# Kernel tuning notes

Hardware: AMD Instinct MI355X
Metric: run time of the kernel (lower is better)

Reference implementation:

```python
import jax, jax.numpy as jnp
import numpy as np
from jax import lax

H = 128  # rec1_size = input_size = hidden_size


def setup_inputs() -> dict:
    key = jax.random.key(0)
    ks = jax.random.split(key, 7)
    B, T = 64, 2048
    x = jax.random.normal(ks[0], (B, T, H), dtype=jnp.float32)
    h0 = jax.random.normal(ks[1], (1, B, H), dtype=jnp.float32)
    c0 = jax.random.normal(ks[2], (1, B, H), dtype=jnp.float32)
    s = 1.0 / np.sqrt(H)  # PyTorch LSTM init: U(-1/sqrt(H), 1/sqrt(H))
    W_ih = jax.random.uniform(ks[3], (4 * H, H), jnp.float32, -s, s)
    W_hh = jax.random.uniform(ks[4], (4 * H, H), jnp.float32, -s, s)
    b_ih = jax.random.uniform(ks[5], (4 * H,), jnp.float32, -s, s)
    b_hh = jax.random.uniform(ks[6], (4 * H,), jnp.float32, -s, s)
    return {"x": x, "h0": h0, "c0": c0, "W_ih": W_ih, "W_hh": W_hh,
            "b_ih": b_ih, "b_hh": b_hh}


def _lstm(x, h0, c0, W_ih, W_hh, b_ih, b_hh):
    # Precompute the input projection for all timesteps in one big GEMM.
    # Gate order in PyTorch: i, f, g, o.
    xg = jnp.einsum('bti,gi->btg', x, W_ih) + b_ih + b_hh  # [B, T, 4H]

    def step(carry, xg_t):
        h, c = carry                       # [B, H], [B, H]
        g = xg_t + h @ W_hh.T              # [B, 4H]
        i = jax.nn.sigmoid(g[:, 0 * H:1 * H])
        f = jax.nn.sigmoid(g[:, 1 * H:2 * H])
        gg = jnp.tanh(g[:, 2 * H:3 * H])
        o = jax.nn.sigmoid(g[:, 3 * H:4 * H])
        c_new = f * c + i * gg
        h_new = o * jnp.tanh(c_new)
        return (h_new, c_new), h_new

    (_, _), hs = lax.scan(step, (h0[0], c0[0]), jnp.swapaxes(xg, 0, 1))
    return jnp.swapaxes(hs, 0, 1)          # [B, T, H]


def reference(x, h0, c0, W_ih, W_hh, b_ih, b_hh):
    # The module's `activation` attribute is never applied in forward();
    # output is the raw LSTM sequence of hidden states.
    return _lstm(x, h0, c0, W_ih, W_hh, b_ih, b_hh)
```

## Files before the change

kernel.cpp:

```cpp
#include <hip/hip_runtime.h>
#include <cstdint>
#include <cmath>


#define HID 128
#define G4  512
#define BB  64
#define TT  2048

typedef float v2f __attribute__((ext_vector_type(2)));
typedef float v4f __attribute__((ext_vector_type(4)));

#define PIN2(v) asm volatile("" : "+v"(v))
#define FMA2(A, B, C) __builtin_elementwise_fma((A), (B), (C))

#define LOG2E  1.442695041f

template<int CTRL>
__device__ __forceinline__ float dpp_mov(float v) {
    return __int_as_float(__builtin_amdgcn_update_dpp(
        0, __float_as_int(v), CTRL, 0xF, 0xF, true));
}
#define BF8(p) { p += dpp_mov<0xB1>(p); p += dpp_mov<0x4E>(p); p += dpp_mov<0x141>(p); }

__global__ __launch_bounds__(512)
__attribute__((amdgpu_waves_per_eu(4, 4)))
void xproj_kernel(const float* __restrict__ x, const float* __restrict__ W_ih,
                  const float* __restrict__ b_ih, const float* __restrict__ b_hh,
                  float* __restrict__ xg, int t0, int Tc) {
    __shared__ __align__(16) v4f xs4[16 * 32];
    const int j    = threadIdx.x;
    const int row0 = blockIdx.x * 16;
    const int b    = row0 / Tc;
    const int tc0  = row0 % Tc;

    const float* xsrc = x + ((size_t)b * TT + (size_t)t0 + tc0) * HID;
    xs4[j] = reinterpret_cast<const v4f*>(xsrc)[j];

    const float bias = b_ih[j] + b_hh[j];
    const v4f* wr4 = reinterpret_cast<const v4f*>(W_ih + (size_t)j * HID);

    v2f wv[32];
    #pragma unroll
    for (int k = 0; k < 16; ++k) {
        const v4f t = wr4[k];
        wv[2 * k] = t.xy; wv[2 * k + 1] = t.zw;
    }
    #pragma unroll
    for (int k = 0; k < 32; ++k) PIN2(wv[k]);
    __syncthreads();

    float acc[16];
    #pragma unroll
    for (int r = 0; r < 16; ++r) {
        const v4f* xp = &xs4[r * 32];
        v2f a0 = {0.f, 0.f}, a1 = {0.f, 0.f};
        #pragma unroll
        for (int k = 0; k < 16; ++k) {
            const v4f v = xp[k];
            a0 = FMA2(wv[2 * k],     v.xy, a0);
            a1 = FMA2(wv[2 * k + 1], v.zw, a1);
        }
        const v2f s = a0 + a1;
        acc[r] = bias + s.x + s.y;
    }
    #pragma unroll
    for (int k = 0; k < 16; ++k) {
        const v4f t = wr4[16 + k];
        wv[2 * k] = t.xy; wv[2 * k + 1] = t.zw;
    }
    #pragma unroll
    for (int k = 0; k < 32; ++k) PIN2(wv[k]);
    #pragma unroll
    for (int r = 0; r < 16; ++r) {
        const v4f* xp = &xs4[r * 32] + 16;
        v2f a0 = {0.f, 0.f}, a1 = {0.f, 0.f};
        #pragma unroll
        for (int k = 0; k < 16; ++k) {
            const v4f v = xp[k];
            a0 = FMA2(wv[2 * k],     v.xy, a0);
            a1 = FMA2(wv[2 * k + 1], v.zw, a1);
        }
        const v2f s = a0 + a1;
        acc[r] += s.x + s.y;
    }

    float* dst = xg + ((size_t)b * Tc + tc0) * G4 + ((j & 127) << 2) + (j >> 7);
    #pragma unroll
    for (int r = 0; r < 16; ++r)
        dst[(size_t)r * G4] = acc[r];
}

__global__ __launch_bounds__(1024)
__attribute__((amdgpu_waves_per_eu(4, 4)))
void lstm_rec_kernel(const float* __restrict__ xg, const float* __restrict__ h0,
                     const float* __restrict__ c0, const float* __restrict__ W_hh,
                     float* __restrict__ out, float* __restrict__ hstate,
                     float* __restrict__ cstate, int t0, int Tc) {
    __shared__ __align__(16) float h_lds[2][160];
    const int t   = threadIdx.x;
    const int g   = t >> 3;
    const int l   = t & 7;
    const int sel = l & 3;
    const int b   = blockIdx.x;

    const float* wl = W_hh + 16 * l;
    v2f W[4][8];
    #pragma unroll
    for (int q = 0; q < 4; ++q) {
        const v4f* wp = reinterpret_cast<const v4f*>(wl + (size_t)(q * 128 + g) * HID);
        #pragma unroll
        for (int k = 0; k < 4; ++k) {
            const v4f tw = wp[k];
            W[q][2 * k] = tw.xy; W[q][2 * k + 1] = tw.zw;
        }
    }
    #pragma unroll
    for (int q = 0; q < 4; ++q)
        #pragma unroll
        for (int k = 0; k < 8; ++k) PIN2(W[q][k]);

    const bool  la   = (l & 1) != 0;
    const bool  lb   = (l & 2) != 0;
    const float negK = (sel == 2) ? -2.f * LOG2E : -LOG2E;
    const float gA   = (sel == 2) ? 2.f : 1.f;
    const float gB   = (sel == 2) ? -1.f : 0.f;

    float c = (t0 == 0) ? c0[b * HID + g] : cstate[b * HID + g];
    if (t < HID) {
        const int pi = 20 * (t >> 4) + (t & 15);
        h_lds[0][pi] = (t0 == 0) ? h0[b * HID + t] : hstate[b * HID + t];
    }
    __syncthreads();

    v2f hcv[8];
    #pragma unroll
    for (int k = 0; k < 4; ++k) {
        const v4f hv = *reinterpret_cast<const v4f*>(&h_lds[0][20 * l + 4 * k]);
        hcv[2 * k] = hv.xy; hcv[2 * k + 1] = hv.zw;
    }

    const float* xq   = xg  + (size_t)b * Tc * G4 + 4 * g + sel;
    float*       outp = out + ((size_t)b * TT + t0) * HID + g;
    float xn = xq[0];

    for (int tc = 0; tc < Tc; ++tc) {
        float xnn = xn;
        if (tc + 1 < Tc)
            xnn = xq[(size_t)(tc + 1) * G4];

        v2f pp0 = {0.f, 0.f}, pp1 = {0.f, 0.f}, pp2 = {0.f, 0.f}, pp3 = {0.f, 0.f};
        #pragma unroll
        for (int k = 0; k < 8; ++k) {
            pp0 = FMA2(W[0][k], hcv[k], pp0);
            pp1 = FMA2(W[1][k], hcv[k], pp1);
            pp2 = FMA2(W[2][k], hcv[k], pp2);
            pp3 = FMA2(W[3][k], hcv[k], pp3);
        }
        float p0 = pp0.x + pp0.y, p1 = pp1.x + pp1.y;
        float p2 = pp2.x + pp2.y, p3 = pp3.x + pp3.y;
        BF8(p0) BF8(p1) BF8(p2) BF8(p3)

        const float t01 = la ? p1 : p0;
        const float t23 = la ? p3 : p2;
        const float xv  = (lb ? t23 : t01) + xn;

        const float e = __builtin_amdgcn_exp2f(xv * negK);
        float r = __builtin_amdgcn_rcpf(1.f + e);
        r = fmaf(r, gA, gB);

        const float vi = dpp_mov<0x00>(r);
        const float vf = dpp_mov<0x55>(r);
        const float vg = dpp_mov<0xAA>(r);
        const float vo = dpp_mov<0xFF>(r);
        c = fmaf(vf, c, vi * vg);
        const float e2 = __builtin_amdgcn_exp2f(c * (-2.f * LOG2E));
        const float th = fmaf(2.f, __builtin_amdgcn_rcpf(1.f + e2), -1.f);
        const float h  = vo * th;

        const int nb = (tc + 1) & 1;
        if (l == 0) {
            h_lds[nb][20 * (g >> 4) + (g & 15)] = h;
            outp[(size_t)tc * HID] = h;
        }
        __syncthreads();
        #pragma unroll
        for (int k = 0; k < 4; ++k) {
            const v4f hv = *reinterpret_cast<const v4f*>(&h_lds[nb][20 * l + 4 * k]);
            hcv[2 * k] = hv.xy; hcv[2 * k + 1] = hv.zw;
        }
        xn = xnn;
    }
    if (l == 0) cstate[b * HID + g] = c;
    if (t < HID) {
        const int pi = 20 * (t >> 4) + (t & 15);
        hstate[b * HID + t] = h_lds[Tc & 1][pi];
    }
}

extern "C" void kernel_launch(void* const* d_in, const int* in_sizes, int n_in,
                              void* d_out, int out_size, void* d_ws, size_t ws_size,
                              hipStream_t stream) {
    const float* x    = (const float*)d_in[0];
    const float* h0   = (const float*)d_in[1];
    const float* c0   = (const float*)d_in[2];
    const float* W_ih = (const float*)d_in[3];
    const float* W_hh = (const float*)d_in[4];
    const float* b_ih = (const float*)d_in[5];
    const float* b_hh = (const float*)d_in[6];
    float* out = (float*)d_out;

    char*  ws     = (char*)d_ws;
    float* hstate = (float*)ws;
    float* cstate = (float*)(ws + 32768);
    float* xg     = (float*)(ws + 65536);

    const size_t per_t = (size_t)BB * G4 * sizeof(float);
    size_t avail = ws_size > 65536 ? ws_size - 65536 : 0;
    long long tc_ll = (long long)(avail / per_t);
    int Tc = tc_ll > TT ? TT : (int)tc_ll;
    Tc = (Tc / 64) * 64;
    if (Tc < 64) Tc = 64;

    for (int t0 = 0; t0 < TT; t0 += Tc) {
        const int Tcur = (TT - t0 < Tc) ? (TT - t0) : Tc;
        xproj_kernel<<<dim3(4 * Tcur), dim3(512), 0, stream>>>(x, W_ih, b_ih, b_hh,
                                                               xg, t0, Tcur);
        lstm_rec_kernel<<<dim3(BB), dim3(1024), 0, stream>>>(xg, h0, c0, W_hh, out,
                                                             hstate, cstate, t0, Tcur);
    }
}
```

Before: 1.719 ms.

## Fuse input projection and recurrence into one persistent kernel with flag-based handoff

```diff
diff --git a/kernel.cpp b/kernel.cpp
--- a/kernel.cpp
+++ b/kernel.cpp
@@ -13,7 +13,6 @@
 
 #define PIN2(v) asm volatile("" : "+v"(v))
 #define FMA2(A, B, C) __builtin_elementwise_fma((A), (B), (C))
-
 #define LOG2E  1.442695041f
 
 template<int CTRL>
@@ -22,6 +21,189 @@
         0, __float_as_int(v), CTRL, 0xF, 0xF, true));
 }
 #define BF8(p) { p += dpp_mov<0xB1>(p); p += dpp_mov<0x4E>(p); p += dpp_mov<0x141>(p); }
+
+__device__ __forceinline__ void xproj_rows16(const v4f* __restrict__ xrows,
+                                             const float* __restrict__ W_ih,
+                                             float bias, int j, float* __restrict__ acc) {
+    const v4f* wr4 = reinterpret_cast<const v4f*>(W_ih + (size_t)j * HID);
+    v2f wv[32];
+    #pragma unroll
+    for (int k = 0; k < 16; ++k) { const v4f t = wr4[k]; wv[2*k] = t.xy; wv[2*k+1] = t.zw; }
+    #pragma unroll
+    for (int k = 0; k < 32; ++k) PIN2(wv[k]);
+    #pragma unroll
+    for (int r = 0; r < 16; ++r) {
+        const v4f* xp = xrows + r * 32;
+        v2f a0 = {0.f,0.f}, a1 = {0.f,0.f};
+        #pragma unroll
+        for (int k = 0; k < 16; ++k) {
+            const v4f v = xp[k];
+            a0 = FMA2(wv[2*k], v.xy, a0); a1 = FMA2(wv[2*k+1], v.zw, a1);
+        }
+        const v2f s = a0 + a1;
+        acc[r] = bias + s.x + s.y;
+    }
+    #pragma unroll
+    for (int k = 0; k < 16; ++k) { const v4f t = wr4[16+k]; wv[2*k] = t.xy; wv[2*k+1] = t.zw; }
+    #pragma unroll
+    for (int k = 0; k < 32; ++k) PIN2(wv[k]);
+    #pragma unroll
+    for (int r = 0; r < 16; ++r) {
+        const v4f* xp = xrows + r * 32 + 16;
+        v2f a0 = {0.f,0.f}, a1 = {0.f,0.f};
+        #pragma unroll
+        for (int k = 0; k < 16; ++k) {
+            const v4f v = xp[k];
+            a0 = FMA2(wv[2*k], v.xy, a0); a1 = FMA2(wv[2*k+1], v.zw, a1);
+        }
+        const v2f s = a0 + a1;
+        acc[r] += s.x + s.y;
+    }
+}
+
+__global__ __launch_bounds__(1024)
+__attribute__((amdgpu_waves_per_eu(4, 4)))
+void lstm_fused_kernel(const float* __restrict__ x, const float* __restrict__ h0,
+                       const float* __restrict__ c0, const float* __restrict__ W_ih,
+                       const float* __restrict__ W_hh, const float* __restrict__ b_ih,
+                       const float* __restrict__ b_hh, float* __restrict__ out,
+                       float* __restrict__ xg, int* __restrict__ flags) {
+    __shared__ __align__(16) float lds_pool[24576];
+    const int t = threadIdx.x;
+
+    if (blockIdx.x >= BB) {
+        const int tile = blockIdx.x - BB;
+        const int bb   = tile & 63;
+        const int w    = tile >> 6;
+        const int tc0  = w * 32;
+        v4f* xs4 = reinterpret_cast<v4f*>(lds_pool);
+        const float* xsrc = x + ((size_t)bb * TT + tc0) * HID;
+        xs4[t] = reinterpret_cast<const v4f*>(xsrc)[t];
+        const int j  = t & 511;
+        const int rg = t >> 9;
+        const float bias = b_ih[j] + b_hh[j];
+        __syncthreads();
+
+        float acc[16];
+        xproj_rows16(xs4 + rg * 16 * 32, W_ih, bias, j, acc);
+
+        float* dst = xg + ((size_t)bb * TT + tc0 + rg * 16) * G4
+                        + ((j & 127) << 2) + (j >> 7);
+        #pragma unroll
+        for (int r = 0; r < 16; ++r)
+            dst[(size_t)r * G4] = acc[r];
+
+        __syncthreads();
+        if (t == 0)
+            __hip_atomic_store(&flags[tile], 1, __ATOMIC_RELEASE,
+                               __HIP_MEMORY_SCOPE_AGENT);
+        return;
+    }
+
+    const int g   = t >> 3;
+    const int l   = t & 7;
+    const int sel = l & 3;
+    const int b   = blockIdx.x;
+    float* hl = lds_pool;
+
+    const float* wl = W_hh + 16 * l;
+    v2f W[4][8];
+    #pragma unroll
+    for (int q = 0; q < 4; ++q) {
+        const v4f* wp = reinterpret_cast<const v4f*>(wl + (size_t)(q * 128 + g) * HID);
+        #pragma unroll
+        for (int k = 0; k < 4; ++k) { const v4f tw = wp[k]; W[q][2*k] = tw.xy; W[q][2*k+1] = tw.zw; }
+    }
+    #pragma unroll
+    for (int q = 0; q < 4; ++q)
+        #pragma unroll
+        for (int k = 0; k < 8; ++k) PIN2(W[q][k]);
+
+    const bool  la   = (l & 1) != 0;
+    const bool  lb   = (l & 2) != 0;
+    const float negK = (sel == 2) ? -2.f * LOG2E : -LOG2E;
+    const float gA   = (sel == 2) ? 2.f : 1.f;
+    const float gB   = (sel == 2) ? -1.f : 0.f;
+
+    float c = c0[b * HID + g];
+    if (t < HID) {
+        const int pi = 20 * (t >> 4) + (t & 15);
+        hl[pi] = h0[b * HID + t];
+    }
+    __syncthreads();
+
+    v2f hcv[8];
+    #pragma unroll
+    for (int k = 0; k < 4; ++k) {
+        const v4f hv = *reinterpret_cast<const v4f*>(&hl[20 * l + 4 * k]);
+        hcv[2*k] = hv.xy; hcv[2*k+1] = hv.zw;
+    }
+
+    #define WAITTILE(idx) { if (t == 0) {                                        \
+        while (__hip_atomic_load(&flags[idx], __ATOMIC_ACQUIRE,                  \
+                                 __HIP_MEMORY_SCOPE_AGENT) == 0)                 \
+            __builtin_amdgcn_s_sleep(8); }                                       \
+        __syncthreads(); }
+    WAITTILE(b)
+    WAITTILE(64 + b)
+
+    const float* xq   = xg  + (size_t)b * TT * G4 + 4 * g + sel;
+    float*       outp = out + (size_t)b * TT * HID + g;
+    float xn = xq[0];
+
+    for (int tc = 0; tc < TT; ++tc) {
+        if ((tc & 31) == 0 && tc != 0) {
+            const int w1 = (tc >> 5) + 1;
+            if (w1 < 64) WAITTILE(w1 * 64 + b)
+        }
+        float xnn = xn;
+        if (tc + 1 < TT)
+            xnn = xq[(size_t)(tc + 1) * G4];
+
+        v2f pp0 = {0.f,0.f}, pp1 = {0.f,0.f}, pp2 = {0.f,0.f}, pp3 = {0.f,0.f};
+        #pragma unroll
+        for (int k = 0; k < 8; ++k) {
+            pp0 = FMA2(W[0][k], hcv[k], pp0);
+            pp1 = FMA2(W[1][k], hcv[k], pp1);
+            pp2 = FMA2(W[2][k], hcv[k], pp2);
+            pp3 = FMA2(W[3][k], hcv[k], pp3);
+        }
+        float p0 = pp0.x + pp0.y, p1 = pp1.x + pp1.y;
+        float p2 = pp2.x + pp2.y, p3 = pp3.x + pp3.y;
+        BF8(p0) BF8(p1) BF8(p2) BF8(p3)
+
+        const float t01 = la ? p1 : p0;
+        const float t23 = la ? p3 : p2;
+        const float xv  = (lb ? t23 : t01) + xn;
+
+        const float e = __builtin_amdgcn_exp2f(xv * negK);
+        float r = __builtin_amdgcn_rcpf(1.f + e);
+        r = fmaf(r, gA, gB);
+
+        const float vi = dpp_mov<0x00>(r);
+        const float vf = dpp_mov<0x55>(r);
+        const float vg = dpp_mov<0xAA>(r);
+        const float vo = dpp_mov<0xFF>(r);
+        c = fmaf(vf, c, vi * vg);
+        const float e2 = __builtin_amdgcn_exp2f(c * (-2.f * LOG2E));
+        const float th = fmaf(2.f, __builtin_amdgcn_rcpf(1.f + e2), -1.f);
+        const float h  = vo * th;
+
+        const int nb = (tc + 1) & 1;
+        if (l == 0) {
+            hl[nb * 160 + 20 * (g >> 4) + (g & 15)] = h;
+            outp[(size_t)tc * HID] = h;
+        }
+        __syncthreads();
+        #pragma unroll
+        for (int k = 0; k < 4; ++k) {
+            const v4f hv = *reinterpret_cast<const v4f*>(&hl[nb * 160 + 20 * l + 4 * k]);
+            hcv[2*k] = hv.xy; hcv[2*k+1] = hv.zw;
+        }
+        xn = xnn;
+    }
+    #undef WAITTILE
+}
 
 __global__ __launch_bounds__(512)
 __attribute__((amdgpu_waves_per_eu(4, 4)))
@@ -33,58 +215,12 @@
     const int row0 = blockIdx.x * 16;
     const int b    = row0 / Tc;
     const int tc0  = row0 % Tc;
-
     const float* xsrc = x + ((size_t)b * TT + (size_t)t0 + tc0) * HID;
     xs4[j] = reinterpret_cast<const v4f*>(xsrc)[j];
-
     const float bias = b_ih[j] + b_hh[j];
-    const v4f* wr4 = reinterpret_cast<const v4f*>(W_ih + (size_t)j * HID);
-
-    v2f wv[32];
-    #pragma unroll
-    for (int k = 0; k < 16; ++k) {
-        const v4f t = wr4[k];
-        wv[2 * k] = t.xy; wv[2 * k + 1] = t.zw;
-    }
-    #pragma unroll
-    for (int k = 0; k < 32; ++k) PIN2(wv[k]);
     __syncthreads();
-
     float acc[16];
-    #pragma unroll
-    for (int r = 0; r < 16; ++r) {
-        const v4f* xp = &xs4[r * 32];
-        v2f a0 = {0.f, 0.f}, a1 = {0.f, 0.f};
-        #pragma unroll
-        for (int k = 0; k < 16; ++k) {
-            const v4f v = xp[k];
-            a0 = FMA2(wv[2 * k],     v.xy, a0);
-            a1 = FMA2(wv[2 * k + 1], v.zw, a1);
-        }
-        const v2f s = a0 + a1;
-        acc[r] = bias + s.x + s.y;
-    }
-    #pragma unroll
-    for (int k = 0; k < 16; ++k) {
-        const v4f t = wr4[16 + k];
-        wv[2 * k] = t.xy; wv[2 * k + 1] = t.zw;
-    }
-    #pragma unroll
-    for (int k = 0; k < 32; ++k) PIN2(wv[k]);
-    #pragma unroll
-    for (int r = 0; r < 16; ++r) {
-        const v4f* xp = &xs4[r * 32] + 16;
-        v2f a0 = {0.f, 0.f}, a1 = {0.f, 0.f};
-        #pragma unroll
-        for (int k = 0; k < 16; ++k) {
-            const v4f v = xp[k];
-            a0 = FMA2(wv[2 * k],     v.xy, a0);
-            a1 = FMA2(wv[2 * k + 1], v.zw, a1);
-        }
-        const v2f s = a0 + a1;
-        acc[r] += s.x + s.y;
-    }
-
+    xproj_rows16(xs4, W_ih, bias, j, acc);
     float* dst = xg + ((size_t)b * Tc + tc0) * G4 + ((j & 127) << 2) + (j >> 7);
     #pragma unroll
     for (int r = 0; r < 16; ++r)
@@ -103,53 +239,43 @@
     const int l   = t & 7;
     const int sel = l & 3;
     const int b   = blockIdx.x;
-
     const float* wl = W_hh + 16 * l;
     v2f W[4][8];
     #pragma unroll
     for (int q = 0; q < 4; ++q) {
         const v4f* wp = reinterpret_cast<const v4f*>(wl + (size_t)(q * 128 + g) * HID);
         #pragma unroll
-        for (int k = 0; k < 4; ++k) {
-            const v4f tw = wp[k];
-            W[q][2 * k] = tw.xy; W[q][2 * k + 1] = tw.zw;
-        }
+        for (int k = 0; k < 4; ++k) { const v4f tw = wp[k]; W[q][2*k] = tw.xy; W[q][2*k+1] = tw.zw; }
     }
     #pragma unroll
     for (int q = 0; q < 4; ++q)
         #pragma unroll
         for (int k = 0; k < 8; ++k) PIN2(W[q][k]);
-
     const bool  la   = (l & 1) != 0;
     const bool  lb   = (l & 2) != 0;
     const float negK = (sel == 2) ? -2.f * LOG2E : -LOG2E;
     const float gA   = (sel == 2) ? 2.f : 1.f;
     const float gB   = (sel == 2) ? -1.f : 0.f;
-
     float c = (t0 == 0) ? c0[b * HID + g] : cstate[b * HID + g];
     if (t < HID) {
         const int pi = 20 * (t >> 4) + (t & 15);
         h_lds[0][pi] = (t0 == 0) ? h0[b * HID + t] : hstate[b * HID + t];
     }
     __syncthreads();
-
     v2f hcv[8];
     #pragma unroll
     for (int k = 0; k < 4; ++k) {
         const v4f hv = *reinterpret_cast<const v4f*>(&h_lds[0][20 * l + 4 * k]);
-        hcv[2 * k] = hv.xy; hcv[2 * k + 1] = hv.zw;
-    }
-
+        hcv[2*k] = hv.xy; hcv[2*k+1] = hv.zw;
+    }
     const float* xq   = xg  + (size_t)b * Tc * G4 + 4 * g + sel;
     float*       outp = out + ((size_t)b * TT + t0) * HID + g;
     float xn = xq[0];
-
     for (int tc = 0; tc < Tc; ++tc) {
         float xnn = xn;
         if (tc + 1 < Tc)
             xnn = xq[(size_t)(tc + 1) * G4];
-
-        v2f pp0 = {0.f, 0.f}, pp1 = {0.f, 0.f}, pp2 = {0.f, 0.f}, pp3 = {0.f, 0.f};
+        v2f pp0 = {0.f,0.f}, pp1 = {0.f,0.f}, pp2 = {0.f,0.f}, pp3 = {0.f,0.f};
         #pragma unroll
         for (int k = 0; k < 8; ++k) {
             pp0 = FMA2(W[0][k], hcv[k], pp0);
@@ -160,15 +286,12 @@
         float p0 = pp0.x + pp0.y, p1 = pp1.x + pp1.y;
         float p2 = pp2.x + pp2.y, p3 = pp3.x + pp3.y;
         BF8(p0) BF8(p1) BF8(p2) BF8(p3)
-
         const float t01 = la ? p1 : p0;
         const float t23 = la ? p3 : p2;
         const float xv  = (lb ? t23 : t01) + xn;
-
         const float e = __builtin_amdgcn_exp2f(xv * negK);
         float r = __builtin_amdgcn_rcpf(1.f + e);
         r = fmaf(r, gA, gB);
-
         const float vi = dpp_mov<0x00>(r);
         const float vf = dpp_mov<0x55>(r);
         const float vg = dpp_mov<0xAA>(r);
@@ -177,7 +300,6 @@
         const float e2 = __builtin_amdgcn_exp2f(c * (-2.f * LOG2E));
         const float th = fmaf(2.f, __builtin_amdgcn_rcpf(1.f + e2), -1.f);
         const float h  = vo * th;
-
         const int nb = (tc + 1) & 1;
         if (l == 0) {
             h_lds[nb][20 * (g >> 4) + (g & 15)] = h;
@@ -187,7 +309,7 @@
         #pragma unroll
         for (int k = 0; k < 4; ++k) {
             const v4f hv = *reinterpret_cast<const v4f*>(&h_lds[nb][20 * l + 4 * k]);
-            hcv[2 * k] = hv.xy; hcv[2 * k + 1] = hv.zw;
+            hcv[2*k] = hv.xy; hcv[2*k+1] = hv.zw;
         }
         xn = xnn;
     }
@@ -213,15 +335,24 @@
     char*  ws     = (char*)d_ws;
     float* hstate = (float*)ws;
     float* cstate = (float*)(ws + 32768);
-    float* xg     = (float*)(ws + 65536);
+    int*   flags  = (int*)  (ws + 65536);
+    float* xg     = (float*)(ws + 98304);
+
+    const size_t xg_full = (size_t)BB * TT * G4 * sizeof(float);
+
+    if (ws_size >= 98304 + xg_full) {
+        hipMemsetAsync(flags, 0, 16384, stream);
+        lstm_fused_kernel<<<dim3(BB + 4096), dim3(1024), 0, stream>>>(
+            x, h0, c0, W_ih, W_hh, b_ih, b_hh, out, xg, flags);
+        return;
+    }
 
     const size_t per_t = (size_t)BB * G4 * sizeof(float);
-    size_t avail = ws_size > 65536 ? ws_size - 65536 : 0;
+    size_t avail = ws_size > 98304 ? ws_size - 98304 : 0;
     long long tc_ll = (long long)(avail / per_t);
     int Tc = tc_ll > TT ? TT : (int)tc_ll;
     Tc = (Tc / 64) * 64;
     if (Tc < 64) Tc = 64;
-
     for (int t0 = 0; t0 < TT; t0 += Tc) {
         const int Tcur = (TT - t0 < Tc) ? (TT - t0) : Tc;
         xproj_kernel<<<dim3(4 * Tcur), dim3(512), 0, stream>>>(x, W_ih, b_ih, b_hh,
```

Measured after the change: 1.674 ms. 2.6% less time.
